# Kernel tuning notes

Hardware: AMD Instinct MI355X
Metric: run time of the kernel (lower is better)

## Reference

```python
import jax, jax.numpy as jnp
import numpy as np

DIM = 1024
BATCH = 16384
NUM_LAYERS = 6
S_E = 0.1   # strength_entail
S_C = 0.1   # strength_contra
S_N = 0.05  # strength_neutral
S_NB = 0.05 # strength_neutral_boost
EPS = 1e-12


def _normalize(x, axis=-1):
    # matches F.normalize: x / max(||x||, eps)
    n = jnp.sqrt(jnp.sum(x * x, axis=axis, keepdims=True))
    return x / jnp.maximum(n, EPS)


def setup_inputs() -> dict:
    key = jax.random.key(0)
    ks = jax.random.split(key, 8)
    return {
        "h0": jax.random.normal(ks[0], (BATCH, DIM), dtype=jnp.float32),
        "W1": jax.random.normal(ks[1], (DIM, DIM), dtype=jnp.float32) * 0.02,
        "b1": jnp.zeros((DIM,), dtype=jnp.float32),
        "W2": jax.random.normal(ks[2], (DIM, DIM), dtype=jnp.float32) * 0.02,
        "b2": jnp.zeros((DIM,), dtype=jnp.float32),
        "anchor_entail": jax.random.normal(ks[3], (DIM,), dtype=jnp.float32),
        "anchor_contra": jax.random.normal(ks[4], (DIM,), dtype=jnp.float32),
        "anchor_neutral": jax.random.normal(ks[5], (DIM,), dtype=jnp.float32),
    }


def reference(h0, W1, b1, W2, b2, anchor_entail, anchor_contra, anchor_neutral):
    # Static collapse with three fixed anchors (rot_rank=0, adaptive_metric=False).
    e_dir = _normalize(anchor_entail, axis=0)   # [D]
    c_dir = _normalize(anchor_contra, axis=0)
    n_dir = _normalize(anchor_neutral, axis=0)

    h = h0
    for _ in range(NUM_LAYERS):
        h_n = _normalize(h)                      # [B, D]
        a_e = h_n @ e_dir                        # [B]
        a_c = h_n @ c_dir
        a_n = h_n @ n_dir
        # divergence_from_alignment: div = 1 - align
        div_e = 1.0 - a_e
        div_c = 1.0 - a_c
        div_n = 1.0 - a_n

        # small MLP update: Linear -> Tanh -> Linear (torch Linear: x @ W.T + b)
        delta = jnp.tanh(h @ W1.T + b1) @ W2.T + b2

        # per-anchor force directions: normalize(h - anchor_dir)
        f_e = _normalize(h - e_dir)
        f_c = _normalize(h - c_dir)
        f_n = _normalize(h - n_dir)

        # boundary_proximity(a_e, a_c): 1 when equidistant from E and C
        boundary = jnp.clip(1.0 - jnp.abs(a_e - a_c), 0.0, 1.0)  # [B]

        h = (h + delta
             - S_E * div_e[:, None] * f_e
             - S_C * div_c[:, None] * f_c
             - S_N * div_n[:, None] * f_n
             - S_NB * boundary[:, None] * f_n)

        # norm clamp at 10 (soft rescale, as in the torch code)
        h_norm = jnp.sqrt(jnp.sum(h * h, axis=-1, keepdims=True))
        h = jnp.where(h_norm > 10.0, h * (10.0 / (h_norm + 1e-8)), h)
    return h
```

## Files before the change

kernel.cpp:

```cpp
#include <hip/hip_runtime.h>
#include <hip/hip_bf16.h>
#include <math.h>

#define DIM 1024
#define BATCH 16384
#define NLAYER 6

typedef __bf16 bf16_t;
typedef __attribute__((ext_vector_type(8))) __bf16 bf16x8;
typedef __attribute__((ext_vector_type(4))) float f32x4;

__device__ __forceinline__ void gload16(const void* g, void* l) {
  __builtin_amdgcn_global_load_lds(
      (const __attribute__((address_space(1))) void*)g,
      (__attribute__((address_space(3))) void*)l, 16, 0, 0);
}

__device__ __forceinline__ float fast_tanh(float x) {
  x = fminf(9.f, fmaxf(-9.f, x));
  const float e = __expf(x + x);
  return (e - 1.f) * __builtin_amdgcn_rcpf(e + 1.f);
}

__device__ __forceinline__ float bf2f(unsigned short u) {
  return __uint_as_float(((unsigned int)u) << 16);
}

template <int MODE>
__global__ __launch_bounds__(512, 2) void gemm_kernel(
    const bf16_t* __restrict__ A, const bf16_t* __restrict__ W,
    const float* __restrict__ bias, bf16_t* __restrict__ outB,
    float* __restrict__ outF, const f32x4* __restrict__ coef,
    const f32x4* __restrict__ colpack, const float* __restrict__ scaleArr,
    const bf16_t* __restrict__ hbIn) {
  __shared__ __align__(16) bf16_t sA[2][256 * 64];
  __shared__ __align__(16) bf16_t sB[2][256 * 64];
  const int tid = threadIdx.x;
  const int w = tid >> 6;
  const int lane = tid & 63;
  const int bm = blockIdx.x * 256;
  const int bn = blockIdx.y * 256;
  const int wm = (w & 1);
  const int wn = (w >> 1);
  const int lm = lane & 15;
  const int lc = lane >> 4;

  f32x4 acc[8][4] = {};

  const int srow = tid >> 3;
  const int swz = ((tid & 7) ^ (srow & 7)) * 8;
  const bf16_t* gA = A + (size_t)(bm + srow) * DIM + swz;
  const bf16_t* gW = W + (size_t)(bn + srow) * DIM + swz;
  char* ldA = (char*)&sA[0][0] + w * 1024;
  char* ldB = (char*)&sB[0][0] + w * 1024;

  const char* rdA = (const char*)&sA[0][0];
  const char* rdB = (const char*)&sB[0][0];
  int aRow[8], bRow[4], chOff[2];
#pragma unroll
  for (int m = 0; m < 8; ++m) aRow[m] = (wm * 128 + m * 16 + lm) * 128;
#pragma unroll
  for (int n = 0; n < 4; ++n) bRow[n] = (wn * 64 + n * 16 + lm) * 128;
#pragma unroll
  for (int kh = 0; kh < 2; ++kh)
    chOff[kh] = ((kh * 4 + lc) ^ (lm & 7)) * 16;

#pragma unroll
  for (int q = 0; q < 4; ++q) {
    gload16(gA + (size_t)q * 64 * DIM, ldA + q * 8192);
    gload16(gW + (size_t)q * 64 * DIM, ldB + q * 8192);
  }
  asm volatile("s_waitcnt vmcnt(0)" ::: "memory");
  __builtin_amdgcn_s_barrier();

  for (int kt = 0; kt < DIM / 64; ++kt) {
    const int cur = kt & 1;
    const char* cA = rdA + cur * 32768;
    const char* cB = rdB + cur * 32768;
    const bool next = (kt + 1) < (DIM / 64);
    const int koff = (kt + 1) * 64;
#pragma unroll
    for (int p = 0; p < 4; ++p) {
      const int mh = p >> 1, nh = p & 1;
      bf16x8 aF[4][2], bF[2][2];
#pragma unroll
      for (int m = 0; m < 4; ++m)
#pragma unroll
        for (int kh = 0; kh < 2; ++kh)
          aF[m][kh] = *(const bf16x8*)(cA + aRow[mh * 4 + m] + chOff[kh]);
#pragma unroll
      for (int n = 0; n < 2; ++n)
#pragma unroll
        for (int kh = 0; kh < 2; ++kh)
          bF[n][kh] = *(const bf16x8*)(cB + bRow[nh * 2 + n] + chOff[kh]);
      if (p == 0 && next) {
        char* d = ldA + (cur ^ 1) * 32768;
#pragma unroll
        for (int q = 0; q < 4; ++q)
          gload16(gA + koff + (size_t)q * 64 * DIM, d + q * 8192);
      }
      if (p == 1 && next) {
        char* d = ldB + (cur ^ 1) * 32768;
#pragma unroll
        for (int q = 0; q < 4; ++q)
          gload16(gW + koff + (size_t)q * 64 * DIM, d + q * 8192);
      }
      __builtin_amdgcn_sched_barrier(0);
      __builtin_amdgcn_s_barrier();
      asm volatile("s_waitcnt lgkmcnt(0)" ::: "memory");
      __builtin_amdgcn_sched_barrier(0);
      __builtin_amdgcn_s_setprio(1);
#pragma unroll
      for (int m = 0; m < 4; ++m)
#pragma unroll
        for (int n = 0; n < 2; ++n)
#pragma unroll
          for (int kh = 0; kh < 2; ++kh)
            acc[mh * 4 + m][nh * 2 + n] =
                __builtin_amdgcn_mfma_f32_16x16x32_bf16(
                    aF[m][kh], bF[n][kh], acc[mh * 4 + m][nh * 2 + n], 0, 0, 0);
      __builtin_amdgcn_s_setprio(0);
      if (p == 3) asm volatile("s_waitcnt vmcnt(0)" ::: "memory");
      __builtin_amdgcn_s_barrier();
    }
  }

  const int r0 = lc << 2;
#pragma unroll
  for (int m = 0; m < 8; ++m) {
    const int rowBase = bm + wm * 128 + m * 16 + r0;
    if constexpr (MODE == 0) {
      float s4[4];
#pragma unroll
      for (int r = 0; r < 4; ++r) s4[r] = scaleArr[rowBase + r];
#pragma unroll
      for (int n = 0; n < 4; ++n) {
        const int col = bn + wn * 64 + n * 16 + lm;
        const float bv = bias[col];
#pragma unroll
        for (int r = 0; r < 4; ++r)
          outB[(size_t)(rowBase + r) * DIM + col] =
              (bf16_t)fast_tanh(s4[r] * acc[m][n][r] + bv);
      }
    } else {
      f32x4 cf[4];
#pragma unroll
      for (int r = 0; r < 4; ++r) cf[r] = coef[rowBase + r];
#pragma unroll
      for (int n = 0; n < 4; ++n) {
        const int col = bn + wn * 64 + n * 16 + lm;
        const f32x4 cp = colpack[col];
#pragma unroll
        for (int r = 0; r < 4; ++r) {
          const size_t idx = (size_t)(rowBase + r) * DIM + col;
          const float hp = (float)hbIn[idx];
          const float v = acc[m][n][r] + cp.w + cf[r].x * cp.x +
                          cf[r].y * cp.y + cf[r].z * cp.z + cf[r].w * hp;
          outB[idx] = (bf16_t)v;
          if constexpr (MODE == 2) outF[idx] = v;
        }
      }
    }
  }
}

template <int IN_FP32>
__global__ __launch_bounds__(256) void stats_kernel(
    const void* __restrict__ src, bf16_t* __restrict__ dstb,
    float* __restrict__ scaleArr, f32x4* __restrict__ coef,
    const float* __restrict__ dirs, int doClamp) {
  const int row = blockIdx.x;
  const int t = threadIdx.x;
  float4 v;
  if constexpr (IN_FP32) {
    v = ((const float4*)src)[(size_t)row * 256 + t];
  } else {
    const ushort4 u = ((const ushort4*)src)[(size_t)row * 256 + t];
    v.x = bf2f(u.x); v.y = bf2f(u.y); v.z = bf2f(u.z); v.w = bf2f(u.w);
  }
  const float4 e = ((const float4*)dirs)[t];
  const float4 c = ((const float4*)dirs)[t + 256];
  const float4 n = ((const float4*)dirs)[t + 512];
  float ss = v.x * v.x + v.y * v.y + v.z * v.z + v.w * v.w;
  float de = v.x * e.x + v.y * e.y + v.z * e.z + v.w * e.w;
  float dc = v.x * c.x + v.y * c.y + v.z * c.z + v.w * c.w;
  float dn = v.x * n.x + v.y * n.y + v.z * n.z + v.w * n.w;
#pragma unroll
  for (int off = 32; off; off >>= 1) {
    ss += __shfl_down(ss, off);
    de += __shfl_down(de, off);
    dc += __shfl_down(dc, off);
    dn += __shfl_down(dn, off);
  }
  __shared__ float red[4][4];
  const int w = t >> 6;
  if ((t & 63) == 0) {
    red[w][0] = ss; red[w][1] = de; red[w][2] = dc; red[w][3] = dn;
  }
  __syncthreads();
  if constexpr (IN_FP32) {
    union { bf16_t b[4]; uint2 u; } pk;
    pk.b[0] = (bf16_t)v.x; pk.b[1] = (bf16_t)v.y;
    pk.b[2] = (bf16_t)v.z; pk.b[3] = (bf16_t)v.w;
    ((uint2*)dstb)[(size_t)row * 256 + t] = pk.u;
  }
  if (t == 0) {
    float S = 0, E = 0, C = 0, N = 0;
#pragma unroll
    for (int i = 0; i < 4; ++i) {
      S += red[i][0]; E += red[i][1]; C += red[i][2]; N += red[i][3];
    }
    const float norm = sqrtf(S);
    float scale = 1.f;
    if (doClamp && norm > 10.f) scale = 10.f / (norm + 1e-8f);
    const float invn = 1.f / fmaxf(norm, 1e-12f);
    const float ae = E * invn;
    const float ac = C * invn;
    const float an = N * invn;
    const float nc = norm * scale;
    const float re = sqrtf(fmaxf(nc * nc - 2.f * nc * ae + 1.f, 0.f));
    const float rc = sqrtf(fmaxf(nc * nc - 2.f * nc * ac + 1.f, 0.f));
    const float rn = sqrtf(fmaxf(nc * nc - 2.f * nc * an + 1.f, 0.f));
    const float boundary = fminf(fmaxf(1.f - fabsf(ae - ac), 0.f), 1.f);
    f32x4 cf;
    cf.x = 0.1f * (1.f - ae) / fmaxf(re, 1e-12f);
    cf.y = 0.1f * (1.f - ac) / fmaxf(rc, 1e-12f);
    cf.z = (0.05f * (1.f - an) + 0.05f * boundary) / fmaxf(rn, 1e-12f);
    cf.w = scale * (1.f - cf.x - cf.y - cf.z);
    coef[row] = cf;
    scaleArr[row] = scale;
  }
}

__global__ __launch_bounds__(256) void finalize_kernel(
    float* __restrict__ outF, const float* __restrict__ scaleArr) {
  const int row = blockIdx.x;
  const int t = threadIdx.x;
  const float s = scaleArr[row];
  float4 v = ((float4*)outF)[(size_t)row * 256 + t];
  v.x *= s; v.y *= s; v.z *= s; v.w *= s;
  ((float4*)outF)[(size_t)row * 256 + t] = v;
}

__global__ __launch_bounds__(256) void prep_dirs(
    const float* __restrict__ ae, const float* __restrict__ ac,
    const float* __restrict__ an, float* __restrict__ dirs) {
  const int t = threadIdx.x;
  const float4 a = ((const float4*)ae)[t];
  const float4 b = ((const float4*)ac)[t];
  const float4 c = ((const float4*)an)[t];
  float sa = a.x * a.x + a.y * a.y + a.z * a.z + a.w * a.w;
  float sb = b.x * b.x + b.y * b.y + b.z * b.z + b.w * b.w;
  float sc = c.x * c.x + c.y * c.y + c.z * c.z + c.w * c.w;
#pragma unroll
  for (int off = 32; off; off >>= 1) {
    sa += __shfl_down(sa, off);
    sb += __shfl_down(sb, off);
    sc += __shfl_down(sc, off);
  }
  __shared__ float red[4][3];
  __shared__ float fin[3];
  const int w = t >> 6;
  if ((t & 63) == 0) { red[w][0] = sa; red[w][1] = sb; red[w][2] = sc; }
  __syncthreads();
  if (t == 0) {
    float x = 0, y = 0, z = 0;
#pragma unroll
    for (int i = 0; i < 4; ++i) { x += red[i][0]; y += red[i][1]; z += red[i][2]; }
    fin[0] = x; fin[1] = y; fin[2] = z;
  }
  __syncthreads();
  const float ia = 1.f / fmaxf(sqrtf(fin[0]), 1e-12f);
  const float ib = 1.f / fmaxf(sqrtf(fin[1]), 1e-12f);
  const float ic = 1.f / fmaxf(sqrtf(fin[2]), 1e-12f);
  float4 oa, ob, oc;
  oa.x = a.x * ia; oa.y = a.y * ia; oa.z = a.z * ia; oa.w = a.w * ia;
  ob.x = b.x * ib; ob.y = b.y * ib; ob.z = b.z * ib; ob.w = b.w * ib;
  oc.x = c.x * ic; oc.y = c.y * ic; oc.z = c.z * ic; oc.w = c.w * ic;
  ((float4*)dirs)[t] = oa;
  ((float4*)dirs)[t + 256] = ob;
  ((float4*)dirs)[t + 512] = oc;
}

__global__ __launch_bounds__(256) void prep_cols(
    const float* __restrict__ dirs, const float* __restrict__ b2,
    f32x4* __restrict__ colpack) {
  const int t = threadIdx.x;
  const float4 e = ((const float4*)dirs)[t];
  const float4 c = ((const float4*)dirs)[t + 256];
  const float4 n = ((const float4*)dirs)[t + 512];
  const float4 b = ((const float4*)b2)[t];
  f32x4 o;
  o.x = e.x; o.y = c.x; o.z = n.x; o.w = b.x; colpack[4 * t + 0] = o;
  o.x = e.y; o.y = c.y; o.z = n.y; o.w = b.y; colpack[4 * t + 1] = o;
  o.x = e.z; o.y = c.z; o.z = n.z; o.w = b.z; colpack[4 * t + 2] = o;
  o.x = e.w; o.y = c.w; o.z = n.w; o.w = b.w; colpack[4 * t + 3] = o;
}

__global__ __launch_bounds__(256) void cast_w_kernel(
    const float* __restrict__ W, bf16_t* __restrict__ Wb) {
  const int i = blockIdx.x * 256 + threadIdx.x;
  const float4 v = ((const float4*)W)[i];
  union { bf16_t b[4]; uint2 u; } pk;
  pk.b[0] = (bf16_t)v.x; pk.b[1] = (bf16_t)v.y;
  pk.b[2] = (bf16_t)v.z; pk.b[3] = (bf16_t)v.w;
  ((uint2*)Wb)[i] = pk.u;
}

extern "C" void kernel_launch(void* const* d_in, const int* in_sizes, int n_in,
                              void* d_out, int out_size, void* d_ws,
                              size_t ws_size, hipStream_t stream) {
  const float* h0 = (const float*)d_in[0];
  const float* W1 = (const float*)d_in[1];
  const float* b1 = (const float*)d_in[2];
  const float* W2 = (const float*)d_in[3];
  const float* b2 = (const float*)d_in[4];
  const float* ae = (const float*)d_in[5];
  const float* ac = (const float*)d_in[6];
  const float* an = (const float*)d_in[7];
  float* outF = (float*)d_out;

  char* ws = (char*)d_ws;
  bf16_t* hb = (bf16_t*)ws;  ws += (size_t)BATCH * DIM * 2;
  bf16_t* Tb = (bf16_t*)ws;  ws += (size_t)BATCH * DIM * 2;
  bf16_t* W1b = (bf16_t*)ws; ws += (size_t)DIM * DIM * 2;
  bf16_t* W2b = (bf16_t*)ws; ws += (size_t)DIM * DIM * 2;
  float* dirs = (float*)ws;  ws += 3 * DIM * 4;
  f32x4* colpack = (f32x4*)ws; ws += DIM * 16;
  f32x4* coef = (f32x4*)ws;  ws += (size_t)BATCH * 16;
  float* scaleArr = (float*)ws; ws += (size_t)BATCH * 4;

  prep_dirs<<<1, 256, 0, stream>>>(ae, ac, an, dirs);
  prep_cols<<<1, 256, 0, stream>>>(dirs, b2, colpack);
  cast_w_kernel<<<DIM * DIM / 1024, 256, 0, stream>>>(W1, W1b);
  cast_w_kernel<<<DIM * DIM / 1024, 256, 0, stream>>>(W2, W2b);
  stats_kernel<1><<<BATCH, 256, 0, stream>>>(h0, hb, scaleArr, coef, dirs, 0);

  dim3 grid(BATCH / 256, DIM / 256);
  for (int l = 0; l < NLAYER; ++l) {
    gemm_kernel<0><<<grid, 512, 0, stream>>>(hb, W1b, b1, Tb, nullptr, nullptr,
                                             nullptr, scaleArr, nullptr);
    if (l < NLAYER - 1) {
      gemm_kernel<1><<<grid, 512, 0, stream>>>(Tb, W2b, b2, hb, nullptr, coef,
                                               colpack, nullptr, hb);
      stats_kernel<0><<<BATCH, 256, 0, stream>>>(hb, nullptr, scaleArr, coef,
                                                 dirs, 1);
    } else {
      gemm_kernel<2><<<grid, 512, 0, stream>>>(Tb, W2b, b2, hb, outF, coef,
                                               colpack, nullptr, hb);
      stats_kernel<0><<<BATCH, 256, 0, stream>>>(hb, nullptr, scaleArr, coef,
                                                 dirs, 1);
      finalize_kernel<<<BATCH, 256, 0, stream>>>(outF, scaleArr);
    }
  }
}
```

Before: 843.9 us.

## Restage GEMM epilogue through LDS for vectorized stores and simplify K-loop

Rewrites the GEMM main loop into one prefetch issue per K-tile with B fragments loaded once and reused across two A halves, replacing the four-phase fine-grained barrier/setprio schedule with a single __syncthreads per tile. The epilogue now transposes accumulators through LDS so each lane writes 16 contiguous columns with 128-bit stores and vector loads of bias, hbIn and the fp32 output. This is meant to cut scattered 2-byte global stores in the epilogue. It risks losing the MFMA/load overlap the previous interleaved schedule provided.

```diff
diff --git a/kernel.cpp b/kernel.cpp
--- a/kernel.cpp
+++ b/kernel.cpp
@@ -33,8 +33,7 @@
     float* __restrict__ outF, const f32x4* __restrict__ coef,
     const f32x4* __restrict__ colpack, const float* __restrict__ scaleArr,
     const bf16_t* __restrict__ hbIn) {
-  __shared__ __align__(16) bf16_t sA[2][256 * 64];
-  __shared__ __align__(16) bf16_t sB[2][256 * 64];
+  __shared__ __align__(16) char smem[131072];
   const int tid = threadIdx.x;
   const int w = tid >> 6;
   const int lane = tid & 63;
@@ -51,114 +50,127 @@
   const int swz = ((tid & 7) ^ (srow & 7)) * 8;
   const bf16_t* gA = A + (size_t)(bm + srow) * DIM + swz;
   const bf16_t* gW = W + (size_t)(bn + srow) * DIM + swz;
-  char* ldA = (char*)&sA[0][0] + w * 1024;
-  char* ldB = (char*)&sB[0][0] + w * 1024;
-
-  const char* rdA = (const char*)&sA[0][0];
-  const char* rdB = (const char*)&sB[0][0];
-  int aRow[8], bRow[4], chOff[2];
-#pragma unroll
-  for (int m = 0; m < 8; ++m) aRow[m] = (wm * 128 + m * 16 + lm) * 128;
-#pragma unroll
-  for (int n = 0; n < 4; ++n) bRow[n] = (wn * 64 + n * 16 + lm) * 128;
-#pragma unroll
-  for (int kh = 0; kh < 2; ++kh)
-    chOff[kh] = ((kh * 4 + lc) ^ (lm & 7)) * 16;
+  char* ldA = smem + w * 1024;
+  char* ldB = smem + 65536 + w * 1024;
+
+  const int aBase = (wm * 128 + lm) * 128;
+  const int bBase = (wn * 64 + lm) * 128;
+  int chOff[2];
+#pragma unroll
+  for (int kh = 0; kh < 2; ++kh) chOff[kh] = ((kh * 4 + lc) ^ (lm & 7)) * 16;
 
 #pragma unroll
   for (int q = 0; q < 4; ++q) {
     gload16(gA + (size_t)q * 64 * DIM, ldA + q * 8192);
     gload16(gW + (size_t)q * 64 * DIM, ldB + q * 8192);
   }
-  asm volatile("s_waitcnt vmcnt(0)" ::: "memory");
-  __builtin_amdgcn_s_barrier();
+  __syncthreads();
 
   for (int kt = 0; kt < DIM / 64; ++kt) {
     const int cur = kt & 1;
-    const char* cA = rdA + cur * 32768;
-    const char* cB = rdB + cur * 32768;
-    const bool next = (kt + 1) < (DIM / 64);
-    const int koff = (kt + 1) * 64;
-#pragma unroll
-    for (int p = 0; p < 4; ++p) {
-      const int mh = p >> 1, nh = p & 1;
-      bf16x8 aF[4][2], bF[2][2];
+    const char* cA = smem + cur * 32768;
+    const char* cB = smem + 65536 + cur * 32768;
+    if (kt + 1 < DIM / 64) {
+      const int koff = (kt + 1) * 64;
+      char* dA = ldA + (cur ^ 1) * 32768;
+      char* dB = ldB + (cur ^ 1) * 32768;
+#pragma unroll
+      for (int q = 0; q < 4; ++q) {
+        gload16(gA + koff + (size_t)q * 64 * DIM, dA + q * 8192);
+        gload16(gW + koff + (size_t)q * 64 * DIM, dB + q * 8192);
+      }
+    }
+    __builtin_amdgcn_sched_barrier(0);
+
+    bf16x8 Bf[4][2];
+#pragma unroll
+    for (int n = 0; n < 4; ++n)
+#pragma unroll
+      for (int kh = 0; kh < 2; ++kh)
+        Bf[n][kh] = *(const bf16x8*)(cB + bBase + n * 2048 + chOff[kh]);
+
+#pragma unroll
+    for (int half = 0; half < 2; ++half) {
+      bf16x8 Af[4][2];
 #pragma unroll
       for (int m = 0; m < 4; ++m)
 #pragma unroll
         for (int kh = 0; kh < 2; ++kh)
-          aF[m][kh] = *(const bf16x8*)(cA + aRow[mh * 4 + m] + chOff[kh]);
-#pragma unroll
-      for (int n = 0; n < 2; ++n)
-#pragma unroll
-        for (int kh = 0; kh < 2; ++kh)
-          bF[n][kh] = *(const bf16x8*)(cB + bRow[nh * 2 + n] + chOff[kh]);
-      if (p == 0 && next) {
-        char* d = ldA + (cur ^ 1) * 32768;
+          Af[m][kh] = *(const bf16x8*)(cA + aBase + (half * 4 + m) * 2048 +
+                                       chOff[kh]);
+#pragma unroll
+      for (int m = 0; m < 4; ++m)
+#pragma unroll
+        for (int n = 0; n < 4; ++n)
+#pragma unroll
+          for (int kh = 0; kh < 2; ++kh)
+            acc[half * 4 + m][n] = __builtin_amdgcn_mfma_f32_16x16x32_bf16(
+                Af[m][kh], Bf[n][kh], acc[half * 4 + m][n], 0, 0, 0);
+    }
+    __syncthreads();
+  }
+
+  float* epi = (float*)(smem + w * 8704);
+  const int r0 = lc << 2;
+  const int rr = lane >> 2;
+  const int cc = (lane & 3) << 4;
+  const int gcol = bn + wn * 64 + cc;
+
+#pragma unroll
+  for (int m = 0; m < 8; ++m) {
+    float* eb = epi + (m & 1) * 1088;
+#pragma unroll
+    for (int n = 0; n < 4; ++n)
+#pragma unroll
+      for (int r = 0; r < 4; ++r)
+        eb[(r0 + r) * 68 + (n << 4) + lm] = acc[m][n][r];
+    asm volatile("s_waitcnt lgkmcnt(0)" ::: "memory");
+    const float* src = eb + rr * 68 + cc;
+    f32x4 v[4];
+#pragma unroll
+    for (int q = 0; q < 4; ++q) v[q] = *(const f32x4*)(src + 4 * q);
+
+    const int grow = bm + wm * 128 + m * 16 + rr;
+    if constexpr (MODE == 0) {
+      const float s = scaleArr[grow];
+      const float* bp = bias + gcol;
+      union { bf16_t b[16]; uint4 u[2]; } pk;
+#pragma unroll
+      for (int q = 0; q < 4; ++q) {
+        const f32x4 bv = *(const f32x4*)(bp + 4 * q);
+#pragma unroll
+        for (int j = 0; j < 4; ++j)
+          pk.b[4 * q + j] = (bf16_t)fast_tanh(s * v[q][j] + bv[j]);
+      }
+      uint4* dst = (uint4*)(outB + (size_t)grow * DIM + gcol);
+      dst[0] = pk.u[0];
+      dst[1] = pk.u[1];
+    } else {
+      const f32x4 cf = coef[grow];
+      const bf16_t* hp = hbIn + (size_t)grow * DIM + gcol;
+      union { bf16_t b[16]; uint4 u[2]; } hin;
+      hin.u[0] = *(const uint4*)hp;
+      hin.u[1] = *(const uint4*)(hp + 8);
+      union { bf16_t b[16]; uint4 u[2]; } pk;
+      f32x4 fo[4];
+#pragma unroll
+      for (int q = 0; q < 4; ++q)
+#pragma unroll
+        for (int j = 0; j < 4; ++j) {
+          const int jj = 4 * q + j;
+          const f32x4 cp = colpack[gcol + jj];
+          const float val = v[q][j] + cp.w + cf.x * cp.x + cf.y * cp.y +
+                            cf.z * cp.z + cf.w * (float)hin.b[jj];
+          pk.b[jj] = (bf16_t)val;
+          fo[q][j] = val;
+        }
+      uint4* dst = (uint4*)(outB + (size_t)grow * DIM + gcol);
+      dst[0] = pk.u[0];
+      dst[1] = pk.u[1];
+      if constexpr (MODE == 2) {
 #pragma unroll
         for (int q = 0; q < 4; ++q)
-          gload16(gA + koff + (size_t)q * 64 * DIM, d + q * 8192);
-      }
-      if (p == 1 && next) {
-        char* d = ldB + (cur ^ 1) * 32768;
-#pragma unroll
-        for (int q = 0; q < 4; ++q)
-          gload16(gW + koff + (size_t)q * 64 * DIM, d + q * 8192);
-      }
-      __builtin_amdgcn_sched_barrier(0);
-      __builtin_amdgcn_s_barrier();
-      asm volatile("s_waitcnt lgkmcnt(0)" ::: "memory");
-      __builtin_amdgcn_sched_barrier(0);
-      __builtin_amdgcn_s_setprio(1);
-#pragma unroll
-      for (int m = 0; m < 4; ++m)
-#pragma unroll
-        for (int n = 0; n < 2; ++n)
-#pragma unroll
-          for (int kh = 0; kh < 2; ++kh)
-            acc[mh * 4 + m][nh * 2 + n] =
-                __builtin_amdgcn_mfma_f32_16x16x32_bf16(
-                    aF[m][kh], bF[n][kh], acc[mh * 4 + m][nh * 2 + n], 0, 0, 0);
-      __builtin_amdgcn_s_setprio(0);
-      if (p == 3) asm volatile("s_waitcnt vmcnt(0)" ::: "memory");
-      __builtin_amdgcn_s_barrier();
-    }
-  }
-
-  const int r0 = lc << 2;
-#pragma unroll
-  for (int m = 0; m < 8; ++m) {
-    const int rowBase = bm + wm * 128 + m * 16 + r0;
-    if constexpr (MODE == 0) {
-      float s4[4];
-#pragma unroll
-      for (int r = 0; r < 4; ++r) s4[r] = scaleArr[rowBase + r];
-#pragma unroll
-      for (int n = 0; n < 4; ++n) {
-        const int col = bn + wn * 64 + n * 16 + lm;
-        const float bv = bias[col];
-#pragma unroll
-        for (int r = 0; r < 4; ++r)
-          outB[(size_t)(rowBase + r) * DIM + col] =
-              (bf16_t)fast_tanh(s4[r] * acc[m][n][r] + bv);
-      }
-    } else {
-      f32x4 cf[4];
-#pragma unroll
-      for (int r = 0; r < 4; ++r) cf[r] = coef[rowBase + r];
-#pragma unroll
-      for (int n = 0; n < 4; ++n) {
-        const int col = bn + wn * 64 + n * 16 + lm;
-        const f32x4 cp = colpack[col];
-#pragma unroll
-        for (int r = 0; r < 4; ++r) {
-          const size_t idx = (size_t)(rowBase + r) * DIM + col;
-          const float hp = (float)hbIn[idx];
-          const float v = acc[m][n][r] + cp.w + cf[r].x * cp.x +
-                          cf[r].y * cp.y + cf[r].z * cp.z + cf[r].w * hp;
-          outB[idx] = (bf16_t)v;
-          if constexpr (MODE == 2) outF[idx] = v;
-        }
+          *(f32x4*)(outF + (size_t)grow * DIM + gcol + 4 * q) = fo[q];
       }
     }
   }
```

Result: slower. 864.5 us (+2.4%).
